# Kernel optimization log

Measured on AMD Instinct MI355X. Metric: run time of the kernel, lower is better.

The kernel has to match this reference:

```python
import jax, jax.numpy as jnp
import numpy as np

N = 20000       # nodes
E = 320000      # edges
IN_C = 256      # in_channels
HID = 256       # hidden_channels
H = 8           # heads
D = HID // H    # head dim = 32
SCALE = 1.0 / np.sqrt(D)
DIN = IN_C + HID


def _lin_params(key, din, dout):
    k1, k2 = jax.random.split(key)
    W = jax.random.normal(k1, (din, dout), jnp.float32) * (1.0 / np.sqrt(din))
    b = jax.random.normal(k2, (dout,), jnp.float32) * 0.01
    return W, b


def setup_inputs() -> dict:
    key = jax.random.key(0)
    ks = jax.random.split(key, 16)
    inp = {
        "x": jax.random.normal(ks[0], (N, IN_C), jnp.float32),
        "h": jax.random.normal(ks[1], (N, HID), jnp.float32) * 0.1,
        "edge_index": jax.random.randint(ks[2], (2, E), 0, N, dtype=jnp.int32),
    }
    i = 3
    for name in ["z", "r", "c"]:
        for p in ["Wq", "Wk", "Wv", "Ws"]:
            W, b = _lin_params(ks[i], DIN, HID)
            i += 1
            inp[f"{name}_{p}"] = W
            inp[f"{name}_b{p[1].lower()}"] = b
    return inp


def _tconv(x, src, dst, Wq, bq, Wk, bk, Wv, bv, Ws, bs):
    """PyG TransformerConv (eval mode, concat=True, root_weight=True, beta=False)."""
    # dense per-node projections, then edge-indexed gathers
    q = (x @ Wq + bq)[dst].reshape(-1, H, D)   # [E, H, D] query at target
    k = (x @ Wk + bk)[src].reshape(-1, H, D)   # [E, H, D] key at source
    v = (x @ Wv + bv)[src].reshape(-1, H, D)   # [E, H, D] value at source
    logits = jnp.sum(q * k, axis=-1) * SCALE   # [E, H]
    # segment softmax over each destination's neighborhood
    m = jax.ops.segment_max(logits, dst, num_segments=N)
    e = jnp.exp(logits - m[dst])
    s = jax.ops.segment_sum(e, dst, num_segments=N)
    alpha = e / (s[dst] + 1e-16)               # [E, H]
    agg = jax.ops.segment_sum(alpha[:, :, None] * v, dst, num_segments=N)
    return agg.reshape(N, HID) + x @ Ws + bs   # attention out + root skip


def reference(x, h, edge_index,
              z_Wq, z_bq, z_Wk, z_bk, z_Wv, z_bv, z_Ws, z_bs,
              r_Wq, r_bq, r_Wk, r_bk, r_Wv, r_bv, r_Ws, r_bs,
              c_Wq, c_bq, c_Wk, c_bk, c_Wv, c_bv, c_Ws, c_bs):
    src, dst = edge_index[0], edge_index[1]
    h_in = jnp.concatenate([x, h], axis=-1)                      # [N, DIN]
    z = jax.nn.sigmoid(_tconv(h_in, src, dst, z_Wq, z_bq, z_Wk, z_bk, z_Wv, z_bv, z_Ws, z_bs))
    r = jax.nn.sigmoid(_tconv(h_in, src, dst, r_Wq, r_bq, r_Wk, r_bk, r_Wv, r_bv, r_Ws, r_bs))
    h_cand = jnp.concatenate([x, r * h], axis=-1)                # [N, DIN]
    h_tilde = jnp.tanh(_tconv(h_cand, src, dst, c_Wq, c_bq, c_Wk, c_bk, c_Wv, c_bv, c_Ws, c_bs))
    return z * h + (1.0 - z) * h_tilde
```

## Files before the change

kernel.cpp:

```cpp
#include <hip/hip_runtime.h>
#include <hip/hip_bf16.h>
#include <math.h>

#define NNODES 20000
#define MPAD 20096
#define NEDGES 320000
#define HIDC 256
#define DINC 512
#define NHEAD 8
#define HDIM 32
#define SCALE 0.17677669529663687f

typedef __attribute__((ext_vector_type(8))) short short8;
typedef __attribute__((ext_vector_type(4))) short svec4;
typedef __attribute__((ext_vector_type(4))) float f32x4;

__device__ __forceinline__ void gload_lds16(const void* g, void* l) {
    __builtin_amdgcn_global_load_lds(
        (const __attribute__((address_space(1))) unsigned int*)g,
        (__attribute__((address_space(3))) unsigned int*)l, 16, 0, 0);
}

__device__ __forceinline__ float bfbits(unsigned short u) {
    return __uint_as_float(((unsigned)u) << 16);
}

__global__ __launch_bounds__(256) void concat_xh(const float* __restrict__ x,
                                                 const float* __restrict__ h,
                                                 __hip_bfloat16* __restrict__ out) {
    int i = blockIdx.x * 256 + threadIdx.x;
    int total = MPAD * DINC;
    if (i >= total) return;
    int row = i >> 9;
    int col = i & 511;
    float v = 0.f;
    if (row < NNODES)
        v = (col < HIDC) ? x[row * HIDC + col] : h[row * HIDC + (col - HIDC)];
    out[i] = __float2bfloat16(v);
}

struct WPtrs { const float* p[12]; };

__global__ __launch_bounds__(256) void transpose_w(WPtrs wp, __hip_bfloat16* __restrict__ out) {
    __shared__ float t[64][65];
    int mat = blockIdx.z;
    int kt = blockIdx.x * 64;
    int nt = blockIdx.y * 64;
    const float* W = wp.p[mat];
    int c = threadIdx.x & 63, r4 = threadIdx.x >> 6;
#pragma unroll
    for (int rr = 0; rr < 16; ++rr) {
        int k_l = r4 + rr * 4;
        t[k_l][c] = W[(kt + k_l) * HIDC + nt + c];
    }
    __syncthreads();
#pragma unroll
    for (int rr = 0; rr < 16; ++rr) {
        int n_l = r4 + rr * 4;
        out[mat * (HIDC * DINC) + (nt + n_l) * DINC + kt + c] =
            __float2bfloat16(t[c][n_l]);
    }
}

__global__ __launch_bounds__(256) void count_deg(const int* __restrict__ dst,
                                                 int* __restrict__ deg) {
    int e = blockIdx.x * 256 + threadIdx.x;
    if (e >= NEDGES) return;
    atomicAdd(&deg[dst[e]], 1);
}

__global__ __launch_bounds__(1024) void exscan(const int* __restrict__ deg,
                                               int* __restrict__ rowptr,
                                               int* __restrict__ pos) {
    __shared__ int sdata[1024];
    __shared__ int s_carry;
    const int tid = threadIdx.x;
    if (tid == 0) { s_carry = 0; rowptr[0] = 0; }
    __syncthreads();
    for (int base = 0; base < NNODES; base += 1024) {
        int i = base + tid;
        int v = (i < NNODES) ? deg[i] : 0;
        sdata[tid] = v;
        __syncthreads();
        for (int off = 1; off < 1024; off <<= 1) {
            int t = (tid >= off) ? sdata[tid - off] : 0;
            __syncthreads();
            sdata[tid] += t;
            __syncthreads();
        }
        int incl = sdata[tid];
        int carry = s_carry;
        if (i < NNODES) {
            int ex = carry + incl - v;
            rowptr[i] = ex;
            pos[i] = ex;
            if (i == NNODES - 1) rowptr[NNODES] = carry + incl;
        }
        __syncthreads();
        if (tid == 1023) s_carry = carry + incl;
        __syncthreads();
    }
}

__global__ __launch_bounds__(256) void scatter_src(const int* __restrict__ src,
                                                   const int* __restrict__ dst,
                                                   int* __restrict__ pos,
                                                   int* __restrict__ csrc) {
    int e = blockIdx.x * 256 + threadIdx.x;
    if (e >= NEDGES) return;
    int idx = atomicAdd(&pos[dst[e]], 1);
    csrc[idx] = src[e];
}

struct GemmArgs { const float* bias[8]; void* C[8]; unsigned bf16mask; };

template <int NZ>
__global__ __launch_bounds__(256) void gemm_mfma(
    const __hip_bfloat16* __restrict__ A,
    const __hip_bfloat16* __restrict__ WtBase,
    GemmArgs ga) {
    __shared__ __align__(16) char smem[2][32768];

    int nwg = gridDim.x;
    int per = nwg >> 3;
    int lin = (blockIdx.x & 7) * per + (blockIdx.x >> 3);
    int bmIdx = lin / NZ;
    int nz = lin % NZ;
    int bm = bmIdx * 128;
    int bn = (nz & 1) * 128;
    int z = nz >> 1;

    const __hip_bfloat16* Bt = WtBase + (size_t)z * (HIDC * DINC);
    const float* bias = ga.bias[z];
    void* Cv = ga.C[z];
    bool isb = (ga.bf16mask >> z) & 1;

    int tid = threadIdx.x;
    int wave = tid >> 6, lane = tid & 63;
    int lrow = lane >> 3;
    int lcol = (lane & 7) ^ lrow;

    int wr = wave >> 1, wc = wave & 1;
    int m_base = wr * 64, n_base = wc * 64;
    int l16 = lane & 15, lk = lane >> 4;

    f32x4 acc[4][4] = {};

    auto stage = [&](int buf, int kt) {
        char* As = smem[buf];
        char* Bs = smem[buf] + 16384;
#pragma unroll
        for (int c4 = 0; c4 < 4; ++c4) {
            int c = wave * 4 + c4;
            gload_lds16(&A[(size_t)(bm + c * 8 + lrow) * DINC + kt + lcol * 8],
                        As + c * 1024);
        }
#pragma unroll
        for (int c4 = 0; c4 < 4; ++c4) {
            int c = wave * 4 + c4;
            gload_lds16(&Bt[(size_t)(bn + c * 8 + lrow) * DINC + kt + lcol * 8],
                        Bs + c * 1024);
        }
    };

    auto compute = [&](int buf) {
        char* As = smem[buf];
        char* Bs = smem[buf] + 16384;
#pragma unroll
        for (int kk = 0; kk < 2; ++kk) {
            short8 af[4], bf[4];
#pragma unroll
            for (int f = 0; f < 4; ++f) {
                int row = m_base + f * 16 + l16;
                int lin2 = row * 128 + (kk * 32 + lk * 8) * 2;
                af[f] = *(const short8*)(As + (lin2 ^ ((row & 7) << 4)));
                int rowb = n_base + f * 16 + l16;
                int linb = rowb * 128 + (kk * 32 + lk * 8) * 2;
                bf[f] = *(const short8*)(Bs + (linb ^ ((rowb & 7) << 4)));
            }
#pragma unroll
            for (int i = 0; i < 4; ++i)
#pragma unroll
                for (int j = 0; j < 4; ++j)
                    acc[i][j] = __builtin_amdgcn_mfma_f32_16x16x32_bf16(
                        af[i], bf[j], acc[i][j], 0, 0, 0);
        }
    };

    stage(0, 0);
#pragma unroll
    for (int t = 0; t < 8; ++t) {
        int cur = t & 1;
        if (t < 7) {
            stage(cur ^ 1, (t + 1) * 64);
            asm volatile("s_waitcnt vmcnt(8)" ::: "memory");
        } else {
            asm volatile("s_waitcnt vmcnt(0)" ::: "memory");
        }
        __builtin_amdgcn_s_barrier();
        __builtin_amdgcn_sched_barrier(0);
        compute(cur);
        __builtin_amdgcn_sched_barrier(0);
        __builtin_amdgcn_s_barrier();
    }

#pragma unroll
    for (int i = 0; i < 4; ++i) {
#pragma unroll
        for (int j = 0; j < 4; ++j) {
            int n = bn + n_base + j * 16 + l16;
            float bia = bias[n];
#pragma unroll
            for (int r = 0; r < 4; ++r) {
                int m = bm + m_base + i * 16 + lk * 4 + r;
                if (m < NNODES) {
                    float val = acc[i][j][r] + bia;
                    if (isb)
                        ((__hip_bfloat16*)Cv)[(size_t)m * HIDC + n] = __float2bfloat16(val);
                    else
                        ((float*)Cv)[(size_t)m * HIDC + n] = val;
                }
            }
        }
    }
}

__global__ __launch_bounds__(256) void attn_zr(
    const __hip_bfloat16* __restrict__ Qz, const __hip_bfloat16* __restrict__ Kz,
    const __hip_bfloat16* __restrict__ Vz, const float* __restrict__ Sz,
    const __hip_bfloat16* __restrict__ Qr, const __hip_bfloat16* __restrict__ Kr,
    const __hip_bfloat16* __restrict__ Vr, const float* __restrict__ Sr,
    const int* __restrict__ rowptr, const int* __restrict__ csrc,
    const float* __restrict__ h,
    float* __restrict__ Zout, __hip_bfloat16* __restrict__ abuf) {
    int lane = threadIdx.x & 63;
    int node = blockIdx.x * 4 + (threadIdx.x >> 6);

    int eA = lane >> 4;
    int gA = (lane >> 3) & 1;
    int hA = lane & 7;
    int gC = lane >> 5;
    int cL = lane & 31;
    int cBase = cL * 8;
    int hC = cL >> 2;
    int wsrc = gC * 8 + hC;

    const __hip_bfloat16* Qa = gA ? Qr : Qz;
    const __hip_bfloat16* Ka = gA ? Kr : Kz;
    const __hip_bfloat16* Vc = gC ? Vr : Vz;

    float qreg[32];
    {
        const short8* Qrow = (const short8*)&Qa[(size_t)node * HIDC + hA * 32];
#pragma unroll
        for (int i = 0; i < 4; ++i) {
            short8 v = Qrow[i];
#pragma unroll
            for (int j = 0; j < 8; ++j)
                qreg[i * 8 + j] = bfbits((unsigned short)v[j]);
        }
    }

    int beg = rowptr[node], end = rowptr[node + 1];
    float acc[8] = {};
    float s_priv = 0.f;

    for (int base = beg; base < end; base += 4) {
        int cnt = min(4, end - base);
        int sn = 0;
        if (lane < cnt) sn = csrc[base + lane];
        int mySn = __shfl(sn, eA);
        float w = 0.f;
        if (eA < cnt) {
            const short8* Krow = (const short8*)&Ka[(size_t)mySn * HIDC + hA * 32];
            float dot = 0.f;
#pragma unroll
            for (int i = 0; i < 4; ++i) {
                short8 kv = Krow[i];
#pragma unroll
                for (int j = 0; j < 8; ++j)
                    dot += qreg[i * 8 + j] * bfbits((unsigned short)kv[j]);
            }
            w = __expf(dot * SCALE);
        }
#pragma unroll 4
        for (int e = 0; e < cnt; ++e) {
            int sne = __shfl(sn, e);
            float we = __shfl(w, e * 16 + wsrc);
            short8 v = *(const short8*)&Vc[(size_t)sne * HIDC + cBase];
#pragma unroll
            for (int j = 0; j < 8; ++j) acc[j] += we * bfbits((unsigned short)v[j]);
            s_priv += we;
        }
    }

    float inv = 1.f / (s_priv + 1e-16f);
    const float* Sx = gC ? Sr : Sz;
    float g[8];
#pragma unroll
    for (int j = 0; j < 8; ++j) {
        float p = acc[j] * inv + Sx[(size_t)node * HIDC + cBase + j];
        g[j] = 1.f / (1.f + __expf(-p));
    }
    if (gC == 0) {
        float* Zp = &Zout[(size_t)node * HIDC + cBase];
#pragma unroll
        for (int j = 0; j < 8; ++j) Zp[j] = g[j];
    } else {
        const float* hp = &h[(size_t)node * HIDC + cBase];
        __hip_bfloat16* ap = &abuf[(size_t)node * DINC + HIDC + cBase];
#pragma unroll
        for (int j = 0; j < 8; ++j) ap[j] = __float2bfloat16(g[j] * hp[j]);
    }
}

__global__ __launch_bounds__(256) void attn_c(
    const __hip_bfloat16* __restrict__ Q, const __hip_bfloat16* __restrict__ K,
    const __hip_bfloat16* __restrict__ V, const float* __restrict__ S,
    const int* __restrict__ rowptr, const int* __restrict__ csrc,
    const float* __restrict__ zbuf, const float* __restrict__ h,
    float* __restrict__ out) {
    int lane = threadIdx.x & 63;
    int node = blockIdx.x * 4 + (threadIdx.x >> 6);

    int eA = lane >> 3;
    int hA = lane & 7;
    int cBase = lane * 4;
    int hC = lane >> 3;

    float qreg[32];
    {
        const short8* Qrow = (const short8*)&Q[(size_t)node * HIDC + hA * 32];
#pragma unroll
        for (int i = 0; i < 4; ++i) {
            short8 v = Qrow[i];
#pragma unroll
            for (int j = 0; j < 8; ++j)
                qreg[i * 8 + j] = bfbits((unsigned short)v[j]);
        }
    }

    int beg = rowptr[node], end = rowptr[node + 1];
    float acc[4] = {};
    float s_priv = 0.f;

    for (int base = beg; base < end; base += 8) {
        int cnt = min(8, end - base);
        int sn = 0;
        if (lane < cnt) sn = csrc[base + lane];
        int mySn = __shfl(sn, eA);
        float w = 0.f;
        if (eA < cnt) {
            const short8* Krow = (const short8*)&K[(size_t)mySn * HIDC + hA * 32];
            float dot = 0.f;
#pragma unroll
            for (int i = 0; i < 4; ++i) {
                short8 kv = Krow[i];
#pragma unroll
                for (int j = 0; j < 8; ++j)
                    dot += qreg[i * 8 + j] * bfbits((unsigned short)kv[j]);
            }
            w = __expf(dot * SCALE);
        }
#pragma unroll 4
        for (int e = 0; e < cnt; ++e) {
            int sne = __shfl(sn, e);
            float we = __shfl(w, e * 8 + hC);
            svec4 v = *(const svec4*)&V[(size_t)sne * HIDC + cBase];
#pragma unroll
            for (int j = 0; j < 4; ++j) acc[j] += we * bfbits((unsigned short)v[j]);
            s_priv += we;
        }
    }

    float inv = 1.f / (s_priv + 1e-16f);
    f32x4 o;
#pragma unroll
    for (int j = 0; j < 4; ++j) {
        float pre = acc[j] * inv + S[(size_t)node * HIDC + cBase + j];
        float ht = tanhf(pre);
        float zz = zbuf[(size_t)node * HIDC + cBase + j];
        float hh = h[(size_t)node * HIDC + cBase + j];
        o[j] = zz * hh + (1.f - zz) * ht;
    }
    *(f32x4*)&out[(size_t)node * HIDC + cBase] = o;
}

extern "C" void kernel_launch(void* const* d_in, const int* in_sizes, int n_in,
                              void* d_out, int out_size, void* d_ws, size_t ws_size,
                              hipStream_t stream) {
    const float* x = (const float*)d_in[0];
    const float* h = (const float*)d_in[1];
    const int* ei = (const int*)d_in[2];
    const float* Wf[3][4];
    const float* B[3][4];
    for (int g = 0; g < 3; ++g)
        for (int p = 0; p < 4; ++p) {
            Wf[g][p] = (const float*)d_in[3 + g * 8 + p * 2];
            B[g][p] = (const float*)d_in[3 + g * 8 + p * 2 + 1];
        }

    char* ws = (char*)d_ws;
    size_t off = 0;
    auto alloc = [&](size_t bytes) {
        void* p = ws + off;
        off = (off + bytes + 255) & ~(size_t)255;
        return p;
    };
    __hip_bfloat16* Abuf = (__hip_bfloat16*)alloc((size_t)MPAD * DINC * 2);
    __hip_bfloat16* Wt = (__hip_bfloat16*)alloc((size_t)12 * HIDC * DINC * 2);
    __hip_bfloat16* Qz = (__hip_bfloat16*)alloc((size_t)NNODES * HIDC * 2);
    __hip_bfloat16* Kz = (__hip_bfloat16*)alloc((size_t)NNODES * HIDC * 2);
    __hip_bfloat16* Vz = (__hip_bfloat16*)alloc((size_t)NNODES * HIDC * 2);
    float* Sz = (float*)alloc((size_t)NNODES * HIDC * 4);
    __hip_bfloat16* Qr = (__hip_bfloat16*)alloc((size_t)NNODES * HIDC * 2);
    __hip_bfloat16* Kr = (__hip_bfloat16*)alloc((size_t)NNODES * HIDC * 2);
    __hip_bfloat16* Vr = (__hip_bfloat16*)alloc((size_t)NNODES * HIDC * 2);
    float* Sr = (float*)alloc((size_t)NNODES * HIDC * 4);
    float* Zb = (float*)alloc((size_t)NNODES * HIDC * 4);
    int* deg = (int*)alloc((size_t)NNODES * 4);
    int* rowptr = (int*)alloc((size_t)(NNODES + 1) * 4);
    int* pos = (int*)alloc((size_t)NNODES * 4);
    int* csrc = (int*)alloc((size_t)NEDGES * 4);

    const int* srcArr = ei;
    const int* dstArr = ei + NEDGES;

    WPtrs wp;
    for (int g = 0; g < 3; ++g)
        for (int p = 0; p < 4; ++p) wp.p[g * 4 + p] = Wf[g][p];

    (void)hipMemsetAsync(deg, 0, NNODES * sizeof(int), stream);
    concat_xh<<<(MPAD * DINC + 255) / 256, 256, 0, stream>>>(x, h, Abuf);
    transpose_w<<<dim3(8, 4, 12), 256, 0, stream>>>(wp, Wt);
    count_deg<<<(NEDGES + 255) / 256, 256, 0, stream>>>(dstArr, deg);
    exscan<<<1, 1024, 0, stream>>>(deg, rowptr, pos);
    scatter_src<<<(NEDGES + 255) / 256, 256, 0, stream>>>(srcArr, dstArr, pos, csrc);

    {
        GemmArgs ga;
        for (int p = 0; p < 4; ++p) { ga.bias[p] = B[0][p]; ga.bias[4 + p] = B[1][p]; }
        ga.C[0] = Qz; ga.C[1] = Kz; ga.C[2] = Vz; ga.C[3] = Sz;
        ga.C[4] = Qr; ga.C[5] = Kr; ga.C[6] = Vr; ga.C[7] = Sr;
        ga.bf16mask = 0x77;
        gemm_mfma<16><<<(MPAD / 128) * 16, 256, 0, stream>>>(Abuf, Wt, ga);
    }
    attn_zr<<<NNODES / 4, 256, 0, stream>>>(Qz, Kz, Vz, Sz, Qr, Kr, Vr, Sr,
                                            rowptr, csrc, h, Zb, Abuf);
    {
        GemmArgs ga;
        for (int p = 0; p < 8; ++p) { ga.bias[p] = B[2][p & 3]; ga.C[p] = nullptr; }
        ga.C[0] = Qz; ga.C[1] = Kz; ga.C[2] = Vz; ga.C[3] = Sz;
        ga.bf16mask = 0x7;
        gemm_mfma<8><<<(MPAD / 128) * 8, 256, 0, stream>>>(
            Abuf, Wt + (size_t)8 * HIDC * DINC, ga);
    }
    attn_c<<<NNODES / 4, 256, 0, stream>>>(Qz, Kz, Vz, Sz, rowptr, csrc,
                                           Zb, h, (float*)d_out);
}
```

Baseline: 418.0 us.

## Interleave z/r K,V rows and double-buffer neighbor gathers in attention kernels

The GEMM now takes a per-output leading dimension, so the z and r key/value projections are written interleaved into 512-wide rows (K2, V2). One source node's z and r data then share a contiguous row for the gather. Both attention kernels are restructured to software-pipeline the edge loop: K and V rows for the next chunk of neighbors are issued into a second register buffer while the current chunk is computed, hiding gather latency. Q is kept as packed bf16 instead of expanded fp32 registers, which lowers register use but adds conversions in the inner loop and raises register pressure from the double buffers.

Result: faster. 400.4 us (-4.2%).

```diff
diff --git a/kernel.cpp b/kernel.cpp
--- a/kernel.cpp
+++ b/kernel.cpp
@@ -112,7 +112,7 @@
     csrc[idx] = src[e];
 }
 
-struct GemmArgs { const float* bias[8]; void* C[8]; unsigned bf16mask; };
+struct GemmArgs { const float* bias[8]; void* C[8]; int ldc[8]; unsigned bf16mask; };
 
 template <int NZ>
 __global__ __launch_bounds__(256) void gemm_mfma(
@@ -133,6 +133,7 @@
     const __hip_bfloat16* Bt = WtBase + (size_t)z * (HIDC * DINC);
     const float* bias = ga.bias[z];
     void* Cv = ga.C[z];
+    int ldc = ga.ldc[z];
     bool isb = (ga.bf16mask >> z) & 1;
 
     int tid = threadIdx.x;
@@ -216,9 +217,9 @@
                 if (m < NNODES) {
                     float val = acc[i][j][r] + bia;
                     if (isb)
-                        ((__hip_bfloat16*)Cv)[(size_t)m * HIDC + n] = __float2bfloat16(val);
+                        ((__hip_bfloat16*)Cv)[(size_t)m * ldc + n] = __float2bfloat16(val);
                     else
-                        ((float*)Cv)[(size_t)m * HIDC + n] = val;
+                        ((float*)Cv)[(size_t)m * ldc + n] = val;
                 }
             }
         }
@@ -226,10 +227,9 @@
 }
 
 __global__ __launch_bounds__(256) void attn_zr(
-    const __hip_bfloat16* __restrict__ Qz, const __hip_bfloat16* __restrict__ Kz,
-    const __hip_bfloat16* __restrict__ Vz, const float* __restrict__ Sz,
-    const __hip_bfloat16* __restrict__ Qr, const __hip_bfloat16* __restrict__ Kr,
-    const __hip_bfloat16* __restrict__ Vr, const float* __restrict__ Sr,
+    const __hip_bfloat16* __restrict__ Qz, const __hip_bfloat16* __restrict__ Qr,
+    const __hip_bfloat16* __restrict__ K2, const __hip_bfloat16* __restrict__ V2,
+    const float* __restrict__ Sz, const float* __restrict__ Sr,
     const int* __restrict__ rowptr, const int* __restrict__ csrc,
     const float* __restrict__ h,
     float* __restrict__ Zout, __hip_bfloat16* __restrict__ abuf) {
@@ -244,53 +244,76 @@
     int cBase = cL * 8;
     int hC = cL >> 2;
     int wsrc = gC * 8 + hC;
+    size_t kOff = (size_t)gA * 256 + hA * 32;
+    size_t vOff = (size_t)gC * 256 + cBase;
 
     const __hip_bfloat16* Qa = gA ? Qr : Qz;
-    const __hip_bfloat16* Ka = gA ? Kr : Kz;
-    const __hip_bfloat16* Vc = gC ? Vr : Vz;
-
-    float qreg[32];
+    short8 qs[4];
     {
         const short8* Qrow = (const short8*)&Qa[(size_t)node * HIDC + hA * 32];
-#pragma unroll
-        for (int i = 0; i < 4; ++i) {
-            short8 v = Qrow[i];
-#pragma unroll
-            for (int j = 0; j < 8; ++j)
-                qreg[i * 8 + j] = bfbits((unsigned short)v[j]);
-        }
+        qs[0] = Qrow[0]; qs[1] = Qrow[1]; qs[2] = Qrow[2]; qs[3] = Qrow[3];
     }
 
     int beg = rowptr[node], end = rowptr[node + 1];
     float acc[8] = {};
     float s_priv = 0.f;
 
-    for (int base = beg; base < end; base += 4) {
-        int cnt = min(4, end - base);
-        int sn = 0;
-        if (lane < cnt) sn = csrc[base + lane];
-        int mySn = __shfl(sn, eA);
+    auto issueKV = [&](int snL, short8* k, short8* v) {
+        int mySn = __shfl(snL, eA);
+        const short8* Kp = (const short8*)&K2[(size_t)mySn * 512 + kOff];
+        k[0] = Kp[0]; k[1] = Kp[1]; k[2] = Kp[2]; k[3] = Kp[3];
+#pragma unroll
+        for (int e = 0; e < 4; ++e) {
+            int sne = __shfl(snL, e);
+            v[e] = *(const short8*)&V2[(size_t)sne * 512 + vOff];
+        }
+    };
+    auto computeC = [&](int snL, int cnt, short8* k, short8* v) {
         float w = 0.f;
         if (eA < cnt) {
-            const short8* Krow = (const short8*)&Ka[(size_t)mySn * HIDC + hA * 32];
             float dot = 0.f;
 #pragma unroll
             for (int i = 0; i < 4; ++i) {
-                short8 kv = Krow[i];
+                short8 kv = k[i], qv = qs[i];
 #pragma unroll
                 for (int j = 0; j < 8; ++j)
-                    dot += qreg[i * 8 + j] * bfbits((unsigned short)kv[j]);
+                    dot += bfbits((unsigned short)qv[j]) * bfbits((unsigned short)kv[j]);
             }
             w = __expf(dot * SCALE);
         }
-#pragma unroll 4
-        for (int e = 0; e < cnt; ++e) {
-            int sne = __shfl(sn, e);
+#pragma unroll
+        for (int e = 0; e < 4; ++e) {
             float we = __shfl(w, e * 16 + wsrc);
-            short8 v = *(const short8*)&Vc[(size_t)sne * HIDC + cBase];
-#pragma unroll
-            for (int j = 0; j < 8; ++j) acc[j] += we * bfbits((unsigned short)v[j]);
-            s_priv += we;
+            if (e < cnt) {
+                short8 vv = v[e];
+#pragma unroll
+                for (int j = 0; j < 8; ++j) acc[j] += we * bfbits((unsigned short)vv[j]);
+                s_priv += we;
+            }
+        }
+    };
+
+    if (beg < end) {
+        short8 kA[4], vA[4], kB[4], vB[4];
+        int baseA = beg;
+        int cntA = min(4, end - baseA);
+        int snLA = (lane < cntA) ? csrc[baseA + lane] : 0;
+        issueKV(snLA, kA, vA);
+        int baseB = baseA + 4, cntB = 0, snLB = 0;
+        if (baseB < end) { cntB = min(4, end - baseB); snLB = (lane < cntB) ? csrc[baseB + lane] : 0; }
+        for (;;) {
+            if (baseB < end) issueKV(snLB, kB, vB);
+            int baseN = baseB + 4, cntN = 0, snLN = 0;
+            if (baseN < end) { cntN = min(4, end - baseN); snLN = (lane < cntN) ? csrc[baseN + lane] : 0; }
+            computeC(snLA, cntA, kA, vA);
+            if (baseB >= end) break;
+            if (baseN < end) issueKV(snLN, kA, vA);
+            int baseN2 = baseN + 4, cntN2 = 0, snLN2 = 0;
+            if (baseN2 < end) { cntN2 = min(4, end - baseN2); snLN2 = (lane < cntN2) ? csrc[baseN2 + lane] : 0; }
+            computeC(snLB, cntB, kB, vB);
+            if (baseN >= end) break;
+            baseA = baseN; cntA = cntN; snLA = snLN;
+            baseB = baseN2; cntB = cntN2; snLB = snLN2;
         }
     }
 
@@ -328,48 +351,73 @@
     int cBase = lane * 4;
     int hC = lane >> 3;
 
-    float qreg[32];
+    short8 qs[4];
     {
         const short8* Qrow = (const short8*)&Q[(size_t)node * HIDC + hA * 32];
-#pragma unroll
-        for (int i = 0; i < 4; ++i) {
-            short8 v = Qrow[i];
-#pragma unroll
-            for (int j = 0; j < 8; ++j)
-                qreg[i * 8 + j] = bfbits((unsigned short)v[j]);
-        }
+        qs[0] = Qrow[0]; qs[1] = Qrow[1]; qs[2] = Qrow[2]; qs[3] = Qrow[3];
     }
 
     int beg = rowptr[node], end = rowptr[node + 1];
     float acc[4] = {};
     float s_priv = 0.f;
 
-    for (int base = beg; base < end; base += 8) {
-        int cnt = min(8, end - base);
-        int sn = 0;
-        if (lane < cnt) sn = csrc[base + lane];
-        int mySn = __shfl(sn, eA);
+    auto issueKV = [&](int snL, short8* k, svec4* v) {
+        int mySn = __shfl(snL, eA);
+        const short8* Kp = (const short8*)&K[(size_t)mySn * HIDC + hA * 32];
+        k[0] = Kp[0]; k[1] = Kp[1]; k[2] = Kp[2]; k[3] = Kp[3];
+#pragma unroll
+        for (int e = 0; e < 8; ++e) {
+            int sne = __shfl(snL, e);
+            v[e] = *(const svec4*)&V[(size_t)sne * HIDC + cBase];
+        }
+    };
+    auto computeC = [&](int snL, int cnt, short8* k, svec4* v) {
         float w = 0.f;
         if (eA < cnt) {
-            const short8* Krow = (const short8*)&K[(size_t)mySn * HIDC + hA * 32];
             float dot = 0.f;
 #pragma unroll
             for (int i = 0; i < 4; ++i) {
-                short8 kv = Krow[i];
+                short8 kv = k[i], qv = qs[i];
 #pragma unroll
                 for (int j = 0; j < 8; ++j)
-                    dot += qreg[i * 8 + j] * bfbits((unsigned short)kv[j]);
+                    dot += bfbits((unsigned short)qv[j]) * bfbits((unsigned short)kv[j]);
             }
             w = __expf(dot * SCALE);
         }
-#pragma unroll 4
-        for (int e = 0; e < cnt; ++e) {
-            int sne = __shfl(sn, e);
+#pragma unroll
+        for (int e = 0; e < 8; ++e) {
             float we = __shfl(w, e * 8 + hC);
-            svec4 v = *(const svec4*)&V[(size_t)sne * HIDC + cBase];
-#pragma unroll
-            for (int j = 0; j < 4; ++j) acc[j] += we * bfbits((unsigned short)v[j]);
-            s_priv += we;
+            if (e < cnt) {
+                svec4 vv = v[e];
+#pragma unroll
+                for (int j = 0; j < 4; ++j) acc[j] += we * bfbits((unsigned short)vv[j]);
+                s_priv += we;
+            }
+        }
+    };
+
+    if (beg < end) {
+        short8 kA[4], kB[4];
+        svec4 vA[8], vB[8];
+        int baseA = beg;
+        int cntA = min(8, end - baseA);
+        int snLA = (lane < cntA) ? csrc[baseA + lane] : 0;
+        issueKV(snLA, kA, vA);
+        int baseB = baseA + 8, cntB = 0, snLB = 0;
+        if (baseB < end) { cntB = min(8, end - baseB); snLB = (lane < cntB) ? csrc[baseB + lane] : 0; }
+        for (;;) {
+            if (baseB < end) issueKV(snLB, kB, vB);
+            int baseN = baseB + 8, cntN = 0, snLN = 0;
+            if (baseN < end) { cntN = min(8, end - baseN); snLN = (lane < cntN) ? csrc[baseN + lane] : 0; }
+            computeC(snLA, cntA, kA, vA);
+            if (baseB >= end) break;
+            if (baseN < end) issueKV(snLN, kA, vA);
+            int baseN2 = baseN + 8, cntN2 = 0, snLN2 = 0;
+            if (baseN2 < end) { cntN2 = min(8, end - baseN2); snLN2 = (lane < cntN2) ? csrc[baseN2 + lane] : 0; }
+            computeC(snLB, cntB, kB, vB);
+            if (baseN >= end) break;
+            baseA = baseN; cntA = cntN; snLA = snLN;
+            baseB = baseN2; cntB = cntN2; snLB = snLN2;
         }
     }
 
@@ -410,12 +458,10 @@
     __hip_bfloat16* Abuf = (__hip_bfloat16*)alloc((size_t)MPAD * DINC * 2);
     __hip_bfloat16* Wt = (__hip_bfloat16*)alloc((size_t)12 * HIDC * DINC * 2);
     __hip_bfloat16* Qz = (__hip_bfloat16*)alloc((size_t)NNODES * HIDC * 2);
-    __hip_bfloat16* Kz = (__hip_bfloat16*)alloc((size_t)NNODES * HIDC * 2);
-    __hip_bfloat16* Vz = (__hip_bfloat16*)alloc((size_t)NNODES * HIDC * 2);
+    __hip_bfloat16* Qr = (__hip_bfloat16*)alloc((size_t)NNODES * HIDC * 2);
+    __hip_bfloat16* K2 = (__hip_bfloat16*)alloc((size_t)NNODES * 512 * 2);
+    __hip_bfloat16* V2 = (__hip_bfloat16*)alloc((size_t)NNODES * 512 * 2);
     float* Sz = (float*)alloc((size_t)NNODES * HIDC * 4);
-    __hip_bfloat16* Qr = (__hip_bfloat16*)alloc((size_t)NNODES * HIDC * 2);
-    __hip_bfloat16* Kr = (__hip_bfloat16*)alloc((size_t)NNODES * HIDC * 2);
-    __hip_bfloat16* Vr = (__hip_bfloat16*)alloc((size_t)NNODES * HIDC * 2);
     float* Sr = (float*)alloc((size_t)NNODES * HIDC * 4);
     float* Zb = (float*)alloc((size_t)NNODES * HIDC * 4);
     int* deg = (int*)alloc((size_t)NNODES * 4);
@@ -440,21 +486,27 @@
     {
         GemmArgs ga;
         for (int p = 0; p < 4; ++p) { ga.bias[p] = B[0][p]; ga.bias[4 + p] = B[1][p]; }
-        ga.C[0] = Qz; ga.C[1] = Kz; ga.C[2] = Vz; ga.C[3] = Sz;
-        ga.C[4] = Qr; ga.C[5] = Kr; ga.C[6] = Vr; ga.C[7] = Sr;
+        ga.C[0] = Qz;        ga.ldc[0] = 256;
+        ga.C[1] = K2;        ga.ldc[1] = 512;
+        ga.C[2] = V2;        ga.ldc[2] = 512;
+        ga.C[3] = Sz;        ga.ldc[3] = 256;
+        ga.C[4] = Qr;        ga.ldc[4] = 256;
+        ga.C[5] = K2 + 256;  ga.ldc[5] = 512;
+        ga.C[6] = V2 + 256;  ga.ldc[6] = 512;
+        ga.C[7] = Sr;        ga.ldc[7] = 256;
         ga.bf16mask = 0x77;
         gemm_mfma<16><<<(MPAD / 128) * 16, 256, 0, stream>>>(Abuf, Wt, ga);
     }
-    attn_zr<<<NNODES / 4, 256, 0, stream>>>(Qz, Kz, Vz, Sz, Qr, Kr, Vr, Sr,
+    attn_zr<<<NNODES / 4, 256, 0, stream>>>(Qz, Qr, K2, V2, Sz, Sr,
                                             rowptr, csrc, h, Zb, Abuf);
     {
         GemmArgs ga;
-        for (int p = 0; p < 8; ++p) { ga.bias[p] = B[2][p & 3]; ga.C[p] = nullptr; }
-        ga.C[0] = Qz; ga.C[1] = Kz; ga.C[2] = Vz; ga.C[3] = Sz;
+        for (int p = 0; p < 8; ++p) { ga.bias[p] = B[2][p & 3]; ga.C[p] = nullptr; ga.ldc[p] = 256; }
+        ga.C[0] = Qz; ga.C[1] = K2; ga.C[2] = V2; ga.C[3] = Sz;
         ga.bf16mask = 0x7;
         gemm_mfma<8><<<(MPAD / 128) * 8, 256, 0, stream>>>(
             Abuf, Wt + (size_t)8 * HIDC * DINC, ga);
     }
-    attn_c<<<NNODES / 4, 256, 0, stream>>>(Qz, Kz, Vz, Sz, rowptr, csrc,
+    attn_c<<<NNODES / 4, 256, 0, stream>>>(Qz, K2, V2, Sz, rowptr, csrc,
                                            Zb, h, (float*)d_out);
 }
```
